# Optimization experiments

Measured on AMD Instinct MI355X. Metric: run time of the kernel, lower is better.

Reference implementation:

```python
import jax, jax.numpy as jnp
import numpy as np

N_CLI, N_AGG, E, D, L = 100000, 1000, 1600000, 128, 3


def setup_inputs() -> dict:
    key = jax.random.key(0)
    ks = jax.random.split(key, 16)
    inp = {
        'x_clients': jax.random.normal(ks[0], (N_CLI, D), jnp.float32),
        'x_agg': jax.random.normal(ks[1], (N_AGG, D), jnp.float32),
        'c2a_src': jax.random.randint(ks[2], (E,), 0, N_CLI, jnp.int32),
        'c2a_dst': jax.random.randint(ks[3], (E,), 0, N_AGG, jnp.int32),
        'a2c_src': jax.random.randint(ks[4], (E,), 0, N_AGG, jnp.int32),
        'a2c_dst': jax.random.randint(ks[5], (E,), 0, N_CLI, jnp.int32),
    }
    s = 1.0 / np.sqrt(D)
    # stacked per-layer SAGE params for each edge type: W_l (on aggregated msg), W_r (on dst), b
    inp['Wl_c2a'] = jax.random.uniform(ks[6], (L, D, D), jnp.float32, -s, s)
    inp['Wr_c2a'] = jax.random.uniform(ks[7], (L, D, D), jnp.float32, -s, s)
    inp['b_c2a'] = jax.random.uniform(ks[8], (L, D), jnp.float32, -s, s)
    inp['Wl_a2c'] = jax.random.uniform(ks[9], (L, D, D), jnp.float32, -s, s)
    inp['Wr_a2c'] = jax.random.uniform(ks[10], (L, D, D), jnp.float32, -s, s)
    inp['b_a2c'] = jax.random.uniform(ks[11], (L, D), jnp.float32, -s, s)
    inp['W_lin'] = jax.random.uniform(ks[12], (D, 1), jnp.float32, -s, s)
    inp['b_lin'] = jax.random.uniform(ks[13], (1,), jnp.float32, -s, s)
    return inp


def _sage(x_src, x_dst, src, dst, Wl, Wr, b, n_dst):
    # mean aggregation of gathered source features onto dst nodes
    msg = x_src[src]                                        # [E, D]
    summed = jax.ops.segment_sum(msg, dst, num_segments=n_dst)
    cnt = jax.ops.segment_sum(jnp.ones((src.shape[0], 1), x_src.dtype), dst, num_segments=n_dst)
    mean = summed / jnp.maximum(cnt, 1.0)
    return mean @ Wl + x_dst @ Wr + b


def _leaky(x):
    return jnp.where(x >= 0, x, 0.1 * x)


def reference(x_clients, x_agg, c2a_src, c2a_dst, a2c_src, a2c_dst,
              Wl_c2a, Wr_c2a, b_c2a, Wl_a2c, Wr_a2c, b_a2c, W_lin, b_lin):
    xc, xa = x_clients, x_agg
    for l in range(L):
        new_a = _sage(xc, xa, c2a_src, c2a_dst, Wl_c2a[l], Wr_c2a[l], b_c2a[l], N_AGG)
        new_c = _sage(xa, xc, a2c_src, a2c_dst, Wl_a2c[l], Wr_a2c[l], b_a2c[l], N_CLI)
        xa, xc = _leaky(new_a), _leaky(new_c)
    return (xc @ W_lin + b_lin).squeeze(1)
```

## Files before the change

kernel.cpp:

```cpp
#include <hip/hip_runtime.h>

#define D      128
#define NCLI   100000
#define NAGG   1000
#define NLAYER 3
#define NBKT   782
#define NRNG   8
#define NBIN   (NAGG * NRNG)
#define RMAGIC 343598u
#define NHIST  512
#define NCVTX  (NCLI * D / 4 / 256)
#define NCVTW  ((NLAYER * D * D + 255) / 256)
#define NROWT  (NCLI / 32)
#define CAP_E  1536

typedef short bf16x8 __attribute__((ext_vector_type(8)));
typedef float f32x16 __attribute__((ext_vector_type(16)));

static __device__ __forceinline__ float leaky(float x) { return x >= 0.f ? x : 0.1f * x; }

static __device__ __forceinline__ unsigned bf16_rn(float f) {
    unsigned u = __float_as_uint(f);
    return (u + 0x7fffu + ((u >> 16) & 1u)) >> 16;
}
static __device__ __forceinline__ float bf_val(unsigned h) { return __uint_as_float(h << 16); }
static __device__ __forceinline__ unsigned pack_bf2(float lo, float hi) {
    return bf16_rn(lo) | (bf16_rn(hi) << 16);
}
static __device__ __forceinline__ float bf_lo(unsigned v) { return __uint_as_float(v << 16); }
static __device__ __forceinline__ float bf_hi(unsigned v) { return __uint_as_float(v & 0xffff0000u); }

__global__ __launch_bounds__(256) void prep(const int* __restrict__ c2a_src,
                                            const int* __restrict__ c2a_dst,
                                            const int* __restrict__ a2c_dst, int E,
                                            int* __restrict__ cnt_ar, int* __restrict__ bcnt,
                                            const float4* __restrict__ X4,
                                            uint2* __restrict__ xhi, uint2* __restrict__ xlo,
                                            const float* __restrict__ W,
                                            unsigned short* __restrict__ Wt) {
    __shared__ int h[NBIN + NBKT];
    int bid = blockIdx.x;
    if (bid < NHIST) {
        for (int i = threadIdx.x; i < NBIN + NBKT; i += 256) h[i] = 0;
        __syncthreads();
        int stride = NHIST * 256;
        for (int e = bid * 256 + threadIdx.x; e < E; e += stride) {
            int s = c2a_src[e];
            int bin = c2a_dst[e] * NRNG + (int)__umulhi((unsigned)s, RMAGIC);
            atomicAdd(&h[bin], 1);
            atomicAdd(&h[NBIN + (a2c_dst[e] >> 7)], 1);
        }
        __syncthreads();
        for (int i = threadIdx.x; i < NBIN; i += 256)
            if (h[i]) atomicAdd(&cnt_ar[i], h[i]);
        for (int i = threadIdx.x; i < NBKT; i += 256)
            if (h[NBIN + i]) atomicAdd(&bcnt[i], h[NBIN + i]);
    } else if (bid < NHIST + NCVTX) {
        int t = (bid - NHIST) * 256 + threadIdx.x;
        float4 f = X4[t];
        unsigned h0 = bf16_rn(f.x), h1 = bf16_rn(f.y), h2 = bf16_rn(f.z), h3 = bf16_rn(f.w);
        xhi[t] = make_uint2(h0 | (h1 << 16), h2 | (h3 << 16));
        xlo[t] = make_uint2(pack_bf2(f.x - bf_val(h0), f.y - bf_val(h1)),
                            pack_bf2(f.z - bf_val(h2), f.w - bf_val(h3)));
    } else {
        int idx = (bid - NHIST - NCVTX) * 256 + threadIdx.x;
        if (idx >= NLAYER * D * D) return;
        int layer = idx >> 14, rem = idx & (D * D - 1);
        int k = rem >> 7, n = rem & 127;
        float w = W[layer * D * D + k * D + n];
        unsigned hh = bf16_rn(w);
        unsigned short* base = Wt + layer * 2 * D * D;
        base[n * D + k] = (unsigned short)hh;
        base[D * D + n * D + k] = (unsigned short)bf16_rn(w - bf_val(hh));
    }
}

__global__ void scan_both(const int* __restrict__ cnt_ar, int* __restrict__ rp_ar,
                          int* __restrict__ cur_ar, const int* __restrict__ bcnt,
                          int* __restrict__ brp, int* __restrict__ bcur) {
    __shared__ int sh[1024];
    int t = threadIdx.x;
    if (blockIdx.x == 0) {
        int v[8];
        int s = 0;
#pragma unroll
        for (int j = 0; j < 8; j++) {
            int idx = t * 8 + j;
            v[j] = (idx < NBIN) ? cnt_ar[idx] : 0;
            s += v[j];
        }
        sh[t] = s;
        __syncthreads();
        for (int off = 1; off < 1024; off <<= 1) {
            int x = (t >= off) ? sh[t - off] : 0;
            __syncthreads();
            sh[t] += x;
            __syncthreads();
        }
        int run = sh[t] - s;
#pragma unroll
        for (int j = 0; j < 8; j++) {
            int idx = t * 8 + j;
            if (idx < NBIN) {
                rp_ar[idx] = run;
                cur_ar[idx] = run;
            }
            run += v[j];
        }
        if (t == 1023) rp_ar[NBIN] = sh[1023];
    } else {
        int v = (t < NBKT) ? bcnt[t] : 0;
        sh[t] = v;
        __syncthreads();
        for (int off = 1; off < 1024; off <<= 1) {
            int x = (t >= off) ? sh[t - off] : 0;
            __syncthreads();
            sh[t] += x;
            __syncthreads();
        }
        if (t == 0) { brp[0] = 0; bcur[0] = 0; }
        if (t < NBKT) {
            brp[t + 1] = sh[t];
            if (t + 1 < NBKT) bcur[t + 1] = sh[t];
        }
    }
}

__global__ __launch_bounds__(1024) void scatter_both(const int* __restrict__ c2a_src,
                                                     const int* __restrict__ c2a_dst,
                                                     const int* __restrict__ a2c_src,
                                                     const int* __restrict__ a2c_dst, int E,
                                                     int* __restrict__ cur_ar,
                                                     int* __restrict__ col_c2a,
                                                     int* __restrict__ bcur,
                                                     int* __restrict__ sorted1) {
    __shared__ int sbuf[2 * NBIN];
    int tid = threadIdx.x;
    if (blockIdx.x < 256) {
        int* h = sbuf;
        int* base = sbuf + NBIN;
        int chunk = (E + 255) / 256;
        int e0 = blockIdx.x * chunk;
        int e1 = min(E, e0 + chunk);
        for (int i = tid; i < NBIN; i += 1024) h[i] = 0;
        __syncthreads();
        for (int e = e0 + tid; e < e1; e += 1024) {
            int s = c2a_src[e];
            atomicAdd(&h[c2a_dst[e] * NRNG + (int)__umulhi((unsigned)s, RMAGIC)], 1);
        }
        __syncthreads();
        for (int i = tid; i < NBIN; i += 1024) {
            int c = h[i];
            base[i] = c ? atomicAdd(&cur_ar[i], c) : 0;
        }
        __syncthreads();
        for (int e = e0 + tid; e < e1; e += 1024) {
            int s = c2a_src[e];
            int bin = c2a_dst[e] * NRNG + (int)__umulhi((unsigned)s, RMAGIC);
            int pos = atomicAdd(&base[bin], 1);
            col_c2a[pos] = s;
        }
    } else {
        int* h = sbuf;
        int* base = sbuf + NBKT;
        int bid = blockIdx.x - 256;
        int chunk = (E + 255) / 256;
        int e0 = bid * chunk;
        int e1 = min(E, e0 + chunk);
        for (int i = tid; i < NBKT; i += 1024) h[i] = 0;
        __syncthreads();
        for (int e = e0 + tid; e < e1; e += 1024) atomicAdd(&h[a2c_dst[e] >> 7], 1);
        __syncthreads();
        for (int i = tid; i < NBKT; i += 1024) {
            int c = h[i];
            base[i] = c ? atomicAdd(&bcur[i], c) : 0;
        }
        __syncthreads();
        for (int e = e0 + tid; e < e1; e += 1024) {
            int d = a2c_dst[e];
            int pos = atomicAdd(&base[d >> 7], 1);
            sorted1[pos] = ((d & 127) << 10) | a2c_src[e];
        }
    }
}

__global__ __launch_bounds__(512) void bucket_csr(const int* __restrict__ brp,
                                                  const int* __restrict__ sorted1,
                                                  int* __restrict__ rp_c,
                                                  int* __restrict__ col) {
    __shared__ int h[128], cur[128];
    int b = blockIdx.x, tid = threadIdx.x;
    if (tid < 128) h[tid] = 0;
    __syncthreads();
    int beg = brp[b], end = brp[b + 1];
    for (int e = beg + tid; e < end; e += 512) atomicAdd(&h[sorted1[e] >> 10], 1);
    __syncthreads();
    if (tid < 128) cur[tid] = h[tid];
    __syncthreads();
    for (int off = 1; off < 128; off <<= 1) {
        int x = 0;
        if (tid < 128 && tid >= off) x = cur[tid - off];
        __syncthreads();
        if (tid < 128) cur[tid] += x;
        __syncthreads();
    }
    if (tid < 128) {
        int start = beg + cur[tid] - h[tid];
        int c = b * 128 + tid;
        if (c < NCLI) rp_c[c] = start;
        cur[tid] = start;
    }
    if (b == NBKT - 1 && tid == 0) rp_c[NCLI] = end;
    __syncthreads();
    for (int e = beg + tid; e < end; e += 512) {
        int p = sorted1[e];
        int pos = atomicAdd(&cur[p >> 10], 1);
        col[pos] = p & 1023;
    }
}


__global__ __launch_bounds__(512) void gather_mean(const unsigned* __restrict__ tbl,
                                                   const int* __restrict__ rp_ar,
                                                   const int* __restrict__ col,
                                                   float* __restrict__ psum) {
    __shared__ float part[4][8][D];
    int quad = blockIdx.x >> 3, r = blockIdx.x & 7;
    int tid = threadIdx.x;
    int a = tid >> 7;
    int sub = (tid >> 4) & 7;
    int sl = tid & 15;
    const uint4* tbl4 = (const uint4*)tbl;
    int agg = quad * 4 + a;
    int bin = agg * NRNG + r;
    int beg = rp_ar[bin], end = rp_ar[bin + 1];
    float f0 = 0, f1 = 0, f2 = 0, f3 = 0, f4 = 0, f5 = 0, f6 = 0, f7 = 0;
    int e = beg + sub;
    for (; e + 8 < end; e += 16) {
        int s0 = col[e];
        int s1 = col[e + 8];
        uint4 v0 = tbl4[(s0 << 4) + sl];
        uint4 v1 = tbl4[(s1 << 4) + sl];
        f0 += bf_lo(v0.x); f1 += bf_hi(v0.x); f2 += bf_lo(v0.y); f3 += bf_hi(v0.y);
        f4 += bf_lo(v0.z); f5 += bf_hi(v0.z); f6 += bf_lo(v0.w); f7 += bf_hi(v0.w);
        f0 += bf_lo(v1.x); f1 += bf_hi(v1.x); f2 += bf_lo(v1.y); f3 += bf_hi(v1.y);
        f4 += bf_lo(v1.z); f5 += bf_hi(v1.z); f6 += bf_lo(v1.w); f7 += bf_hi(v1.w);
    }
    if (e < end) {
        int s0 = col[e];
        uint4 v0 = tbl4[(s0 << 4) + sl];
        f0 += bf_lo(v0.x); f1 += bf_hi(v0.x); f2 += bf_lo(v0.y); f3 += bf_hi(v0.y);
        f4 += bf_lo(v0.z); f5 += bf_hi(v0.z); f6 += bf_lo(v0.w); f7 += bf_hi(v0.w);
    }
    float* pr = &part[a][sub][sl * 8];
    pr[0] = f0; pr[1] = f1; pr[2] = f2; pr[3] = f3;
    pr[4] = f4; pr[5] = f5; pr[6] = f6; pr[7] = f7;
    __syncthreads();
    int c = tid & 127;
    float s = 0.f;
#pragma unroll
    for (int g = 0; g < 8; g++) s += part[a][g][c];
    psum[((size_t)agg * NRNG + r) * D + c] = s;
}

__global__ __launch_bounds__(128) void combine_agg(const float* __restrict__ psum,
                                                   const int* __restrict__ rp_ar,
                                                   const float* xa_old,
                                                   const float* __restrict__ Wl_a2c,
                                                   const float* __restrict__ Wl_c2a,
                                                   const float* __restrict__ Wr_c2a,
                                                   const float* __restrict__ b_c2a,
                                                   unsigned short* __restrict__ ya_bf,
                                                   float* xa_out) {
    __shared__ float mr[D], xr[D];
    int i = blockIdx.x, j = threadIdx.x;
    const float* pr = psum + (size_t)i * NRNG * D + j;
    float s = 0.f;
#pragma unroll
    for (int r = 0; r < NRNG; r++) s += pr[r * D];
    int deg = rp_ar[i * NRNG + NRNG] - rp_ar[i * NRNG];
    mr[j] = s / fmaxf((float)deg, 1.f);
    xr[j] = xa_old[i * D + j];
    __syncthreads();
    float accy = 0.f, accn = b_c2a[j];
#pragma unroll 4
    for (int k = 0; k < D; k++) {
        accy += xr[k] * Wl_a2c[k * D + j];
        accn += mr[k] * Wl_c2a[k * D + j] + xr[k] * Wr_c2a[k * D + j];
    }
    ya_bf[i * D + j] = (unsigned short)bf16_rn(accy);
    xa_out[i * D + j] = leaky(accn);
}

template <int LAST>
__global__ __launch_bounds__(256) void gemm_agg(const unsigned short* __restrict__ Ahi,
                                                const unsigned short* __restrict__ Alo,
                                                const unsigned short* __restrict__ Wt,
                                                const float* __restrict__ bias,
                                                const unsigned* __restrict__ ya,
                                                const int* __restrict__ rowptr,
                                                const int* __restrict__ col,
                                                unsigned* __restrict__ xhi,
                                                unsigned* __restrict__ xlo,
                                                const float* __restrict__ Wlin,
                                                const float* __restrict__ blin,
                                                float* __restrict__ out, int E) {
    __shared__ float smem[32][D];
    __shared__ int lcol[CAP_E];
    __shared__ int lrp[33];
    int tid = threadIdx.x;
    int wave = tid >> 6, lane = tid & 63;
    int cl = lane & 31, kh = lane >> 5;
    int n0 = wave * 32;
    int m0 = blockIdx.x * 32;
    int blkBeg = rowptr[m0], blkEnd = rowptr[m0 + 32];
    int nE = blkEnd - blkBeg;
    bool inlds = (nE <= CAP_E);
    int pv[6];
#pragma unroll
    for (int k = 0; k < 6; k++) pv[k] = col[min(blkBeg + tid + k * 256, E - 1)];
    if (tid < 33) lrp[tid] = rowptr[m0 + tid];
    float bv = bias[n0 + cl];
    f32x16 acc1;
#pragma unroll
    for (int qq = 0; qq < 16; qq++) acc1[qq] = bv;
    {
        const unsigned short* Wlo_ = Wt + D * D;
        const unsigned short* ar = Ahi + (size_t)(m0 + cl) * D + kh * 8;
        const unsigned short* al = Alo + (size_t)(m0 + cl) * D + kh * 8;
        const unsigned short* wh = Wt + (size_t)(n0 + cl) * D + kh * 8;
        const unsigned short* wl = Wlo_ + (size_t)(n0 + cl) * D + kh * 8;
        if (inlds) {
#pragma unroll
            for (int k = 0; k < 6; k++) lcol[tid + k * 256] = pv[k];
        }
#pragma unroll
        for (int kc = 0; kc < 8; kc++) {
            bf16x8 ahi = *(const bf16x8*)(ar + kc * 16);
            bf16x8 alo = *(const bf16x8*)(al + kc * 16);
            bf16x8 bh = *(const bf16x8*)(wh + kc * 16);
            bf16x8 bl = *(const bf16x8*)(wl + kc * 16);
            acc1 = __builtin_amdgcn_mfma_f32_32x32x16_bf16(ahi, bh, acc1, 0, 0, 0);
            acc1 = __builtin_amdgcn_mfma_f32_32x32x16_bf16(alo, bh, acc1, 0, 0, 0);
            acc1 = __builtin_amdgcn_mfma_f32_32x32x16_bf16(ahi, bl, acc1, 0, 0, 0);
        }
    }
#pragma unroll
    for (int reg = 0; reg < 16; reg++) {
        int row = (reg & 3) + 8 * (reg >> 2) + 4 * kh;
        smem[row][n0 + cl] = acc1[reg];
    }
    __syncthreads();
    const int w8 = wave * 8;
    int e0 = lrp[w8], eend = lrp[w8 + 8];
    int cli = 0;
    int nb = lrp[w8 + 1];
    float s0 = 0.f, s1 = 0.f;
    float wl0 = 0.f, wl1 = 0.f;
    if (LAST) { float2 wv = *(const float2*)&Wlin[2 * lane]; wl0 = wv.x; wl1 = wv.y; }
    auto flushc = [&]() {
        int c_local = w8 + cli;
        int gid = m0 + c_local;
        int deg = lrp[c_local + 1] - lrp[c_local];
        float inv = 1.f / fmaxf((float)deg, 1.f);
        float2 yv = *(const float2*)&smem[c_local][2 * lane];
        float r0 = leaky(yv.x + s0 * inv);
        float r1 = leaky(yv.y + s1 * inv);
        if (LAST) {
            float v = r0 * wl0 + r1 * wl1;
#pragma unroll
            for (int off = 32; off > 0; off >>= 1) v += __shfl_down(v, off);
            if (lane == 0) out[gid] = v + blin[0];
        } else {
            unsigned h0 = bf16_rn(r0), h1 = bf16_rn(r1);
            xhi[(gid << 6) + lane] = h0 | (h1 << 16);
            xlo[(gid << 6) + lane] = pack_bf2(r0 - bf_val(h0), r1 - bf_val(h1));
        }
        s0 = 0.f;
        s1 = 0.f;
    };
    unsigned va[16], vb[16];
    auto loadch = [&](unsigned (&buf)[16], int base) {
        int pos = min(base + (lane & 15), eend - 1);
        int ecs = inlds ? lcol[pos - blkBeg] : col[pos];
#pragma unroll
        for (int j = 0; j < 16; j++) {
            int ec = __shfl(ecs, j);
            buf[j] = ya[(ec << 6) + lane];
        }
    };
    auto consume = [&](unsigned (&buf)[16], int ck) {
#pragma unroll
        for (int j = 0; j < 16; j++) {
            if (ck + j < eend) {
                while (ck + j == nb) {
                    flushc();
                    cli++;
                    nb = lrp[w8 + cli + 1];
                }
                s0 += bf_lo(buf[j]);
                s1 += bf_hi(buf[j]);
            }
        }
    };
    if (e0 < eend) {
        loadch(va, e0);
        for (int ck = e0; ck < eend; ck += 32) {
            if (ck + 16 < eend) loadch(vb, ck + 16);
            consume(va, ck);
            if (ck + 16 < eend) {
                if (ck + 32 < eend) loadch(va, ck + 32);
                consume(vb, ck + 16);
            }
        }
    }
    while (cli < 8) {
        flushc();
        cli++;
    }
}

extern "C" void kernel_launch(void* const* d_in, const int* in_sizes, int n_in,
                              void* d_out, int out_size, void* d_ws, size_t ws_size,
                              hipStream_t stream) {
    const float* x_clients = (const float*)d_in[0];
    const float* x_agg     = (const float*)d_in[1];
    const int*   c2a_src   = (const int*)d_in[2];
    const int*   c2a_dst   = (const int*)d_in[3];
    const int*   a2c_src   = (const int*)d_in[4];
    const int*   a2c_dst   = (const int*)d_in[5];
    const float* Wl_c2a    = (const float*)d_in[6];
    const float* Wr_c2a    = (const float*)d_in[7];
    const float* b_c2a     = (const float*)d_in[8];
    const float* Wl_a2c    = (const float*)d_in[9];
    const float* Wr_a2c    = (const float*)d_in[10];
    const float* b_a2c     = (const float*)d_in[11];
    const float* W_lin     = (const float*)d_in[12];
    const float* b_lin     = (const float*)d_in[13];
    float* out = (float*)d_out;
    const int E = in_sizes[2];

    char* p = (char*)d_ws;
    auto alloc = [&](size_t bytes) {
        char* r = p;
        p += (bytes + 255) & ~(size_t)255;
        return r;
    };
    float*    Yb    = (float*)alloc(sizeof(float) * NCLI * D);
    unsigned* xc_hi = (unsigned*)alloc(sizeof(unsigned) * NCLI * 64);
    unsigned* xc_lo = (unsigned*)alloc(sizeof(unsigned) * NCLI * 64);
    float*    xa    = (float*)alloc(sizeof(float) * NAGG * D);
    unsigned short* ya_bf = (unsigned short*)alloc(sizeof(unsigned short) * NAGG * D);
    unsigned short* Wt = (unsigned short*)alloc(sizeof(unsigned short) * NLAYER * 2 * D * D);
    float* psum  = (float*)alloc(sizeof(float) * NAGG * NRNG * D);
    int* cnt_ar = (int*)alloc(sizeof(int) * (NBIN + NBKT));
    int* bcnt  = cnt_ar + NBIN;
    int* rp_ar = (int*)alloc(sizeof(int) * (NBIN + 1));
    int* cur_ar = (int*)alloc(sizeof(int) * NBIN);
    int* brp   = (int*)alloc(sizeof(int) * (NBKT + 1));
    int* bcur  = (int*)alloc(sizeof(int) * NBKT);
    int* rp_c  = (int*)alloc(sizeof(int) * (NCLI + 1));
    int* col_c2a = (int*)alloc(sizeof(int) * E);
    int* col_a2c = (int*)alloc(sizeof(int) * E);
    int* sorted1 = (int*)Yb;

    hipMemsetAsync(cnt_ar, 0, sizeof(int) * (NBIN + NBKT), stream);

    prep<<<NHIST + NCVTX + NCVTW, 256, 0, stream>>>(c2a_src, c2a_dst, a2c_dst, E, cnt_ar, bcnt,
                                                    (const float4*)x_clients,
                                                    (uint2*)xc_hi, (uint2*)xc_lo,
                                                    Wr_a2c, Wt);
    scan_both<<<2, 1024, 0, stream>>>(cnt_ar, rp_ar, cur_ar, bcnt, brp, bcur);
    scatter_both<<<512, 1024, 0, stream>>>(c2a_src, c2a_dst, a2c_src, a2c_dst, E,
                                           cur_ar, col_c2a, bcur, sorted1);
    bucket_csr<<<NBKT, 512, 0, stream>>>(brp, sorted1, rp_c, col_a2c);

    const float* xa_old = x_agg;
    for (int l = 0; l < NLAYER; l++) {
        gather_mean<<<(NAGG / 4) * NRNG, 512, 0, stream>>>(xc_hi, rp_ar, col_c2a, psum);
        combine_agg<<<NAGG, 128, 0, stream>>>(psum, rp_ar, xa_old,
                                              Wl_a2c + l * D * D, Wl_c2a + l * D * D,
                                              Wr_c2a + l * D * D, b_c2a + l * D, ya_bf, xa);
        if (l < NLAYER - 1) {
            gemm_agg<0><<<NROWT, 256, 0, stream>>>(
                (const unsigned short*)xc_hi, (const unsigned short*)xc_lo,
                Wt + l * 2 * D * D, b_a2c + l * D, (const unsigned*)ya_bf, rp_c, col_a2c,
                xc_hi, xc_lo, nullptr, nullptr, nullptr, E);
        } else {
            gemm_agg<1><<<NROWT, 256, 0, stream>>>(
                (const unsigned short*)xc_hi, (const unsigned short*)xc_lo,
                Wt + l * 2 * D * D, b_a2c + l * D, (const unsigned*)ya_bf, rp_c, col_a2c,
                nullptr, nullptr, W_lin, b_lin, out, E);
        }
        xa_old = xa;
    }
}
```

Baseline: 650.0 us.

## Stage gathered neighbor rows via direct global-to-LDS loads with double buffering

Replaces the register-based gather of neighbor feature rows (16-wide chunks loaded through shuffled indices) with global_load_lds instructions that write straight into a per-wave LDS double buffer of 8 rows, using explicit vmcnt waits. The aim is to cut VGPR pressure and keep more gather loads in flight while the previous chunk is summed. It adds LDS traffic and manual waitcnt handling, and the smaller chunk depth may reduce memory-level parallelism.

Result: slower. 861.7 us (+32.6%).

```diff
diff --git a/kernel.cpp b/kernel.cpp
--- a/kernel.cpp
+++ b/kernel.cpp
@@ -16,6 +16,9 @@
 
 typedef short bf16x8 __attribute__((ext_vector_type(8)));
 typedef float f32x16 __attribute__((ext_vector_type(16)));
+
+typedef __attribute__((address_space(1))) const unsigned g_u32;
+typedef __attribute__((address_space(3))) unsigned l_u32;
 
 static __device__ __forceinline__ float leaky(float x) { return x >= 0.f ? x : 0.1f * x; }
 
@@ -306,6 +309,7 @@
                                                 const float* __restrict__ blin,
                                                 float* __restrict__ out, int E) {
     __shared__ float smem[32][D];
+    __shared__ unsigned abuf[4][2][8][64];
     __shared__ int lcol[CAP_E];
     __shared__ int lrp[33];
     int tid = threadIdx.x;
@@ -379,38 +383,53 @@
         s0 = 0.f;
         s1 = 0.f;
     };
-    unsigned va[16], vb[16];
-    auto loadch = [&](unsigned (&buf)[16], int base) {
-        int pos = min(base + (lane & 15), eend - 1);
-        int ecs = inlds ? lcol[pos - blkBeg] : col[pos];
-#pragma unroll
-        for (int j = 0; j < 16; j++) {
-            int ec = __shfl(ecs, j);
-            buf[j] = ya[(ec << 6) + lane];
+    auto stage = [&](int b, int base) {
+        asm volatile("s_waitcnt lgkmcnt(0)" ::: "memory");
+#pragma unroll
+        for (int j = 0; j < 8; j++) {
+            int e = min(base + j, eend - 1);
+            int idx = inlds ? lcol[e - blkBeg] : col[e];
+            __builtin_amdgcn_global_load_lds((g_u32*)(ya + (idx << 6) + lane),
+                                             (l_u32*)&abuf[wave][b][j][0], 4, 0, 0);
         }
     };
-    auto consume = [&](unsigned (&buf)[16], int ck) {
-#pragma unroll
-        for (int j = 0; j < 16; j++) {
+    auto consume = [&](int b, int ck) {
+#pragma unroll
+        for (int j = 0; j < 8; j++) {
             if (ck + j < eend) {
                 while (ck + j == nb) {
                     flushc();
                     cli++;
                     nb = lrp[w8 + cli + 1];
                 }
-                s0 += bf_lo(buf[j]);
-                s1 += bf_hi(buf[j]);
+                unsigned v = abuf[wave][b][j][lane];
+                s0 += bf_lo(v);
+                s1 += bf_hi(v);
             }
         }
     };
     if (e0 < eend) {
-        loadch(va, e0);
-        for (int ck = e0; ck < eend; ck += 32) {
-            if (ck + 16 < eend) loadch(vb, ck + 16);
-            consume(va, ck);
-            if (ck + 16 < eend) {
-                if (ck + 32 < eend) loadch(va, ck + 32);
-                consume(vb, ck + 16);
+        stage(0, e0);
+        for (int ck = e0; ck < eend; ck += 16) {
+            bool hasB = (ck + 8 < eend);
+            if (hasB) {
+                stage(1, ck + 8);
+                asm volatile("s_waitcnt vmcnt(8)" ::: "memory");
+            } else {
+                asm volatile("s_waitcnt vmcnt(0)" ::: "memory");
+            }
+            __builtin_amdgcn_sched_barrier(0);
+            consume(0, ck);
+            if (hasB) {
+                bool hasA2 = (ck + 16 < eend);
+                if (hasA2) {
+                    stage(0, ck + 16);
+                    asm volatile("s_waitcnt vmcnt(8)" ::: "memory");
+                } else {
+                    asm volatile("s_waitcnt vmcnt(0)" ::: "memory");
+                }
+                __builtin_amdgcn_sched_barrier(0);
+                consume(1, ck + 8);
             }
         }
     }
```
